# Kernel tuning notes

Measured on AMD Instinct MI355X. Metric: run time of the kernel, lower is better.

The kernel has to match this reference:

```python
import jax, jax.numpy as jnp
import numpy as np

B, G, T = 4096, 100, 24


def _greedy_dispatch(demand, caps, prices, slack_price):
    """Exact LP solution of: min prices@alloc + slack_price*slack
    s.t. 0<=alloc<=caps, sum(alloc)+slack = demand (per b,t).
    demand: [B,T] (nonneg), caps: [B,G,T], prices: [G], slack_price: scalar.
    Returns alloc [B,G,T], slack [B,T].
    """
    prices_all = jnp.concatenate([prices, slack_price[None]])        # [G+1]
    # slack capacity = demand itself (slack alone can absorb everything)
    caps_all = jnp.concatenate([caps, demand[:, None, :]], axis=1)    # [B,G+1,T]
    order = jnp.argsort(prices_all)                                   # merit order
    caps_s = caps_all[:, order, :]
    before = jnp.cumsum(caps_s, axis=1) - caps_s                      # capacity ahead in merit order
    alloc_s = jnp.clip(demand[:, None, :] - before, 0.0, caps_s)
    inv = jnp.argsort(order)
    alloc = alloc_s[:, inv, :]
    return alloc[:, :-1, :], alloc[:, -1, :]


def setup_inputs() -> dict:
    key = jax.random.key(0)
    k1, k2, k3, k4 = jax.random.split(key, 4)
    R_up = jax.random.uniform(k1, (B, G, T), dtype=jnp.float32)
    R_dn = jax.random.uniform(k2, (B, G, T), dtype=jnp.float32)
    omega_true = jax.random.normal(k3, (B, T), dtype=jnp.float32) * 5.0
    b_G = 10.0 + 40.0 * jax.random.uniform(k4, (G,), dtype=jnp.float32)  # marginal costs $/MWh
    return {
        "R_up": R_up,
        "R_dn": R_dn,
        "omega_true": omega_true,
        "b_G": b_G,
        "voll": jnp.float32(1000.0),
        "vosp": jnp.float32(500.0),
        "rt_up_ratio": jnp.float32(1.5),
        "rt_dn_ratio": jnp.float32(1.2),
    }


def reference(R_up, R_dn, omega_true, b_G, voll, vosp, rt_up_ratio, rt_dn_ratio):
    c_up = rt_up_ratio * b_G                                          # [G]
    c_dn = rt_dn_ratio * b_G                                          # [G]
    dem_up = jnp.maximum(omega_true, 0.0)                             # [B,T]
    dem_dn = jnp.maximum(-omega_true, 0.0)
    du, LS = _greedy_dispatch(dem_up, R_up, c_up, voll)
    dd, SP = _greedy_dispatch(dem_dn, R_dn, c_dn, vosp)
    rt_obj = (jnp.einsum('g,bgt->b', c_up, du)
              + jnp.einsum('g,bgt->b', c_dn, dd)
              + voll * LS.sum(axis=1) + vosp * SP.sum(axis=1))        # [B]
    return du, dd, LS, SP, rt_obj
```

## Files before the change

### kernel.cpp

```cpp
#include <hip/hip_runtime.h>

#define G_ 100
#define T_ 24
#define GP1 101
#define TILE (G_ * T_)
#define VPB (TILE / 4)
#define WPB 4
#define BLOCK (64 * WPB)

typedef float vfloat4 __attribute__((ext_vector_type(4)));

__global__ void setup_sort_kernel(const float* __restrict__ b_G,
                                  const float* __restrict__ voll,
                                  const float* __restrict__ vosp,
                                  const float* __restrict__ ru,
                                  const float* __restrict__ rd,
                                  int* __restrict__ order_out,
                                  float* __restrict__ price_out)
{
    __shared__ float pu[GP1], pd[GP1];
    int i = threadIdx.x;
    if (i < GP1) {
        if (i < G_) { float bg = b_G[i]; pu[i] = ru[0] * bg; pd[i] = rd[0] * bg; }
        else        { pu[i] = voll[0];   pd[i] = vosp[0]; }
    }
    __syncthreads();
    if (i < GP1) {
        float mu = pu[i], md = pd[i];
        int r0 = 0, r1 = 0;
        for (int j = 0; j < GP1; ++j) {
            float vu = pu[j], vd = pd[j];
            r0 += (vu < mu) || (vu == mu && j < i);
            r1 += (vd < md) || (vd == md && j < i);
        }
        order_out[r0] = i;        price_out[r0] = mu;
        order_out[GP1 + r1] = i;  price_out[GP1 + r1] = md;
    }
}

template<int N>
__device__ __forceinline__ void scan_chunk(int k0,
    const float* __restrict__ capp,
    const int* __restrict__ ordp, const float* __restrict__ prp,
    float* __restrict__ ldscol,
    float dem, float& before, float& objp)
{
    int gg[N]; float pr[N], cap[N];
#pragma unroll
    for (int j = 0; j < N; ++j) { gg[j] = ordp[k0 + j]; pr[j] = prp[k0 + j]; }
#pragma unroll
    for (int j = 0; j < N; ++j) cap[j] = capp[gg[j] * T_];
#pragma unroll
    for (int j = 0; j < N; ++j) {
        float a = fminf(fmaxf(dem - before, 0.f), cap[j]);
        before += cap[j];
        objp = fmaf(pr[j], a, objp);
        ldscol[gg[j] * T_] = a;
    }
}

__global__ __launch_bounds__(BLOCK, 4) void dispatch_kernel(
    const float* __restrict__ R_up, const float* __restrict__ R_dn,
    const float* __restrict__ omega,
    const int* __restrict__ ord_ws, const float* __restrict__ pr_ws,
    float* __restrict__ out, int B)
{
    __shared__ float s_tile[WPB * TILE];
    __shared__ float s_obj[WPB];

    const int tid  = threadIdx.x;
    const int w    = tid >> 6;
    const int lane = tid & 63;
    const int b = __builtin_amdgcn_readfirstlane(blockIdx.x * 2 + (w >> 1));
    const int p = __builtin_amdgcn_readfirstlane(w & 1);
    const size_t bgt = (size_t)B * TILE;
    float* __restrict__ tw = &s_tile[w * TILE];

#pragma unroll
    for (int j = 0; j < 9; ++j) *(vfloat4*)&tw[(lane + j * 64) * 4] = (vfloat4)(0.f);
    if (lane < VPB - 576)       *(vfloat4*)&tw[(lane + 576) * 4]    = (vfloat4)(0.f);

    const int t = (lane < T_) ? lane : 0;
    const int*   __restrict__ ordp = ord_ws + p * GP1;
    const float* __restrict__ prp  = pr_ws  + p * GP1;

    float objp = 0.f;
    if (lane < T_) {
        const float om  = omega[(size_t)b * T_ + t];
        const float dem = p ? fmaxf(-om, 0.f) : fmaxf(om, 0.f);
        const float* __restrict__ capp = (p ? R_dn : R_up) + (size_t)b * TILE + t;
        float* __restrict__ ldscol = tw + t;

        float before = 0.f;
        bool run = true;
        int k = 0;
        for (int c = 0; c < 12 && run; ++c) {
            scan_chunk<8>(k, capp, ordp, prp, ldscol, dem, before, objp);
            k += 8;
            run = __any(before < dem);
        }
        if (run)
            scan_chunk<4>(96, capp, ordp, prp, ldscol, dem, before, objp);

        float slackv = fmaxf(dem - before, 0.f);
        objp = fmaf(prp[GP1 - 1], slackv, objp);
        out[2 * bgt + (size_t)p * B * T_ + (size_t)b * T_ + t] = slackv;
    }

#pragma unroll
    for (int off = 32; off; off >>= 1) objp += __shfl_xor(objp, off, 64);
    if (lane == 0) s_obj[w] = objp;

    __builtin_amdgcn_wave_barrier();
    {
        vfloat4* __restrict__ dst = (vfloat4*)out + ((size_t)p * B + b) * VPB;
#pragma unroll
        for (int j = 0; j < 9; ++j)
            dst[lane + j * 64] = *(const vfloat4*)&tw[(lane + j * 64) * 4];
        if (lane < VPB - 576)
            dst[lane + 576] = *(const vfloat4*)&tw[(lane + 576) * 4];
    }

    __syncthreads();
    if (tid == 0)
        out[2 * bgt + 2 * (size_t)B * T_ + b]     = s_obj[0] + s_obj[1];
    if (tid == 128)
        out[2 * bgt + 2 * (size_t)B * T_ + b]     = s_obj[2] + s_obj[3];
}

extern "C" void kernel_launch(void* const* d_in, const int* in_sizes, int n_in,
                              void* d_out, int out_size, void* d_ws, size_t ws_size,
                              hipStream_t stream)
{
    const float* R_up  = (const float*)d_in[0];
    const float* R_dn  = (const float*)d_in[1];
    const float* omega = (const float*)d_in[2];
    const float* b_G   = (const float*)d_in[3];
    const float* voll  = (const float*)d_in[4];
    const float* vosp  = (const float*)d_in[5];
    const float* ru    = (const float*)d_in[6];
    const float* rd    = (const float*)d_in[7];

    const int B = in_sizes[0] / TILE;
    float* out = (float*)d_out;

    int*   ord_ws = (int*)d_ws;
    float* pr_ws  = (float*)((char*)d_ws + 2 * GP1 * sizeof(int));

    setup_sort_kernel<<<1, 128, 0, stream>>>(b_G, voll, vosp, ru, rd, ord_ws, pr_ws);

    dispatch_kernel<<<B / 2, BLOCK, 0, stream>>>(
        R_up, R_dn, omega, ord_ws, pr_ws, out, B);
}
```

Before: 152.6 us.

## Fuse merit-order sort into dispatch kernel and widen first scan chunk

Removes the separate single-block sort kernel and recomputes the price ranking per block in shared memory, eliminating a launch and the dependency between kernels. Order and prices are read from LDS and made wave-uniform via readfirstlane. The scan now starts with a 24-wide chunk followed by progressively smaller chunks, so more capacity loads are in flight before the first early-exit check. The cost is redundant O(G^2) ranking work and two extra block barriers in every block.

```diff
diff --git a/kernel.cpp b/kernel.cpp
--- a/kernel.cpp
+++ b/kernel.cpp
@@ -10,46 +10,23 @@
 
 typedef float vfloat4 __attribute__((ext_vector_type(4)));
 
-__global__ void setup_sort_kernel(const float* __restrict__ b_G,
-                                  const float* __restrict__ voll,
-                                  const float* __restrict__ vosp,
-                                  const float* __restrict__ ru,
-                                  const float* __restrict__ rd,
-                                  int* __restrict__ order_out,
-                                  float* __restrict__ price_out)
-{
-    __shared__ float pu[GP1], pd[GP1];
-    int i = threadIdx.x;
-    if (i < GP1) {
-        if (i < G_) { float bg = b_G[i]; pu[i] = ru[0] * bg; pd[i] = rd[0] * bg; }
-        else        { pu[i] = voll[0];   pd[i] = vosp[0]; }
-    }
-    __syncthreads();
-    if (i < GP1) {
-        float mu = pu[i], md = pd[i];
-        int r0 = 0, r1 = 0;
-        for (int j = 0; j < GP1; ++j) {
-            float vu = pu[j], vd = pd[j];
-            r0 += (vu < mu) || (vu == mu && j < i);
-            r1 += (vd < md) || (vd == md && j < i);
-        }
-        order_out[r0] = i;        price_out[r0] = mu;
-        order_out[GP1 + r1] = i;  price_out[GP1 + r1] = md;
-    }
-}
-
 template<int N>
-__device__ __forceinline__ void scan_chunk(int k0,
+__device__ __forceinline__ void scan_chunk(int k0, int p,
     const float* __restrict__ capp,
-    const int* __restrict__ ordp, const float* __restrict__ prp,
+    const int* __restrict__ s_ord, const float* __restrict__ s_praw,
     float* __restrict__ ldscol,
     float dem, float& before, float& objp)
 {
     int gg[N]; float pr[N], cap[N];
 #pragma unroll
-    for (int j = 0; j < N; ++j) { gg[j] = ordp[k0 + j]; pr[j] = prp[k0 + j]; }
+    for (int j = 0; j < N; ++j)
+        gg[j] = __builtin_amdgcn_readfirstlane(s_ord[p * GP1 + k0 + j]);
 #pragma unroll
     for (int j = 0; j < N; ++j) cap[j] = capp[gg[j] * T_];
+#pragma unroll
+    for (int j = 0; j < N; ++j)
+        pr[j] = __int_as_float(__builtin_amdgcn_readfirstlane(
+                    ((const int*)s_praw)[p * GP1 + gg[j]]));
 #pragma unroll
     for (int j = 0; j < N; ++j) {
         float a = fminf(fmaxf(dem - before, 0.f), cap[j]);
@@ -61,11 +38,14 @@
 
 __global__ __launch_bounds__(BLOCK, 4) void dispatch_kernel(
     const float* __restrict__ R_up, const float* __restrict__ R_dn,
-    const float* __restrict__ omega,
-    const int* __restrict__ ord_ws, const float* __restrict__ pr_ws,
+    const float* __restrict__ omega, const float* __restrict__ b_G,
+    const float* __restrict__ voll, const float* __restrict__ vosp,
+    const float* __restrict__ ru, const float* __restrict__ rd,
     float* __restrict__ out, int B)
 {
     __shared__ float s_tile[WPB * TILE];
+    __shared__ float s_praw[2 * GP1];
+    __shared__ int   s_ord[2 * GP1];
     __shared__ float s_obj[WPB];
 
     const int tid  = threadIdx.x;
@@ -76,34 +56,66 @@
     const size_t bgt = (size_t)B * TILE;
     float* __restrict__ tw = &s_tile[w * TILE];
 
+    if (tid < GP1) {
+        if (tid < G_) {
+            float bg = b_G[tid];
+            s_praw[tid]       = ru[0] * bg;
+            s_praw[GP1 + tid] = rd[0] * bg;
+        } else {
+            s_praw[tid]       = voll[0];
+            s_praw[GP1 + tid] = vosp[0];
+        }
+    }
+
+    const int t = (lane < T_) ? lane : 0;
+    float om = 0.f;
+    if (lane < T_) om = omega[(size_t)b * T_ + t];
+
 #pragma unroll
     for (int j = 0; j < 9; ++j) *(vfloat4*)&tw[(lane + j * 64) * 4] = (vfloat4)(0.f);
     if (lane < VPB - 576)       *(vfloat4*)&tw[(lane + 576) * 4]    = (vfloat4)(0.f);
+    __syncthreads();
 
-    const int t = (lane < T_) ? lane : 0;
-    const int*   __restrict__ ordp = ord_ws + p * GP1;
-    const float* __restrict__ prp  = pr_ws  + p * GP1;
+    if (tid < GP1) {
+        float mu = s_praw[tid], md = s_praw[GP1 + tid];
+        int r0 = 0, r1 = 0;
+        for (int j = 0; j < GP1; ++j) {
+            float vu = s_praw[j], vd = s_praw[GP1 + j];
+            r0 += (vu < mu) || (vu == mu && j < tid);
+            r1 += (vd < md) || (vd == md && j < tid);
+        }
+        s_ord[r0]       = tid;
+        s_ord[GP1 + r1] = tid;
+    }
+    __syncthreads();
 
     float objp = 0.f;
     if (lane < T_) {
-        const float om  = omega[(size_t)b * T_ + t];
         const float dem = p ? fmaxf(-om, 0.f) : fmaxf(om, 0.f);
         const float* __restrict__ capp = (p ? R_dn : R_up) + (size_t)b * TILE + t;
         float* __restrict__ ldscol = tw + t;
 
         float before = 0.f;
-        bool run = true;
-        int k = 0;
-        for (int c = 0; c < 12 && run; ++c) {
-            scan_chunk<8>(k, capp, ordp, prp, ldscol, dem, before, objp);
-            k += 8;
-            run = __any(before < dem);
-        }
-        if (run)
-            scan_chunk<4>(96, capp, ordp, prp, ldscol, dem, before, objp);
+        scan_chunk<24>( 0, p, capp, s_ord, s_praw, ldscol, dem, before, objp);
+        bool run = __any(before < dem);
+        if (run) { scan_chunk<16>(24, p, capp, s_ord, s_praw, ldscol, dem, before, objp);
+                   run = __any(before < dem); }
+        if (run) { scan_chunk<16>(40, p, capp, s_ord, s_praw, ldscol, dem, before, objp);
+                   run = __any(before < dem); }
+        if (run) { scan_chunk< 8>(56, p, capp, s_ord, s_praw, ldscol, dem, before, objp);
+                   run = __any(before < dem); }
+        if (run) { scan_chunk< 8>(64, p, capp, s_ord, s_praw, ldscol, dem, before, objp);
+                   run = __any(before < dem); }
+        if (run) { scan_chunk< 8>(72, p, capp, s_ord, s_praw, ldscol, dem, before, objp);
+                   run = __any(before < dem); }
+        if (run) { scan_chunk< 8>(80, p, capp, s_ord, s_praw, ldscol, dem, before, objp);
+                   run = __any(before < dem); }
+        if (run) { scan_chunk< 8>(88, p, capp, s_ord, s_praw, ldscol, dem, before, objp);
+                   run = __any(before < dem); }
+        if (run)   scan_chunk< 4>(96, p, capp, s_ord, s_praw, ldscol, dem, before, objp);
 
         float slackv = fmaxf(dem - before, 0.f);
-        objp = fmaf(prp[GP1 - 1], slackv, objp);
+        objp = fmaf(s_praw[p * GP1 + G_], slackv, objp);
         out[2 * bgt + (size_t)p * B * T_ + (size_t)b * T_ + t] = slackv;
     }
 
@@ -123,9 +135,9 @@
 
     __syncthreads();
     if (tid == 0)
-        out[2 * bgt + 2 * (size_t)B * T_ + b]     = s_obj[0] + s_obj[1];
+        out[2 * bgt + 2 * (size_t)B * T_ + b] = s_obj[0] + s_obj[1];
     if (tid == 128)
-        out[2 * bgt + 2 * (size_t)B * T_ + b]     = s_obj[2] + s_obj[3];
+        out[2 * bgt + 2 * (size_t)B * T_ + b] = s_obj[2] + s_obj[3];
 }
 
 extern "C" void kernel_launch(void* const* d_in, const int* in_sizes, int n_in,
@@ -144,11 +156,6 @@
     const int B = in_sizes[0] / TILE;
     float* out = (float*)d_out;
 
-    int*   ord_ws = (int*)d_ws;
-    float* pr_ws  = (float*)((char*)d_ws + 2 * GP1 * sizeof(int));
-
-    setup_sort_kernel<<<1, 128, 0, stream>>>(b_G, voll, vosp, ru, rd, ord_ws, pr_ws);
-
     dispatch_kernel<<<B / 2, BLOCK, 0, stream>>>(
-        R_up, R_dn, omega, ord_ws, pr_ws, out, B);
+        R_up, R_dn, omega, b_G, voll, vosp, ru, rd, out, B);
 }
```

New measurement: 155.9 us. 2.2% more time.
